# Performance work log

Measured on AMD Instinct MI355X. Metric: run time of the kernel, lower is better.

Reference implementation:

```python
import jax, jax.numpy as jnp
import numpy as np

N_HEAD = 16

def setup_inputs() -> dict:
    key = jax.random.key(0)
    k1, k2, k3 = jax.random.split(key, 3)
    B, T, C = 2, 2048, 1024
    x_norm_for_qk = jax.random.normal(k1, (B, T, C), dtype=jnp.float32)
    xt_current_for_v = jax.random.normal(k2, (B, T, C), dtype=jnp.float32)
    W_attn = jax.random.normal(k3, (C, 2 * C), dtype=jnp.float32) * (1.0 / np.sqrt(C))
    b_attn = jnp.zeros((2 * C,), dtype=jnp.float32)
    return {"x_norm_for_qk": x_norm_for_qk, "xt_current_for_v": xt_current_for_v,
            "W_attn": W_attn, "b_attn": b_attn}

def reference(x_norm_for_qk, xt_current_for_v, W_attn, b_attn):
    B, T, C = x_norm_for_qk.shape
    H = N_HEAD
    D = C // H  # head dim
    qk = x_norm_for_qk @ W_attn + b_attn          # [B,T,2C]
    q, k = qk[..., :C], qk[..., C:]
    q = q.reshape(B, T, H, D).transpose(0, 2, 1, 3)   # [B,H,T,D]
    k = k.reshape(B, T, H, D).transpose(0, 2, 1, 3)
    v = xt_current_for_v.reshape(B, T, H, D).transpose(0, 2, 1, 3)
    scale = 1.0 / np.sqrt(D).astype(np.float32)
    scores = jnp.einsum('bhqd,bhkd->bhqk', q, k) * scale  # [B,H,T,T]
    causal = jnp.tril(jnp.ones((T, T), dtype=bool))
    scores = jnp.where(causal[None, None], scores, jnp.float32(-jnp.inf))
    weights = jax.nn.softmax(scores, axis=-1)  # dropout p=0.0 -> identity
    y = jnp.einsum('bhqk,bhkd->bhqd', weights, v)
    return y.transpose(0, 2, 1, 3).reshape(B, T, C)
```

## Files before the change

kernel.cpp:

```cpp
#include <hip/hip_runtime.h>
#include <hip/hip_bf16.h>
#include <math.h>

typedef __attribute__((ext_vector_type(8))) short s8v;
typedef __attribute__((ext_vector_type(4))) float f4v;
typedef __attribute__((ext_vector_type(16))) float f16v;
typedef __attribute__((ext_vector_type(2))) unsigned int u32x2;
typedef unsigned short ush;
typedef unsigned int u32;

#define QSCALE 0.180336880f
#define FIXED_M 10.0f

static __device__ __forceinline__ ush f2bf(float f) {
    u32 x = __builtin_bit_cast(u32, f);
    return (ush)((x + 0x7fffu + ((x >> 16) & 1u)) >> 16);
}
static __device__ __forceinline__ u32 bfpack(float lo, float hi) {
    u32 a = __builtin_bit_cast(u32, lo) + 0x8000u;
    u32 b = __builtin_bit_cast(u32, hi) + 0x8000u;
    return __builtin_amdgcn_perm(b, a, 0x07060302);
}
static __device__ __forceinline__ void gl_lds16(const void* g, void* l) {
    __builtin_amdgcn_global_load_lds(
        (const __attribute__((address_space(1))) u32*)g,
        (__attribute__((address_space(3))) u32*)l, 16, 0, 0);
}
#if __has_builtin(__builtin_amdgcn_exp2f)
#define EXP2F(x) __builtin_amdgcn_exp2f(x)
#else
#define EXP2F(x) exp2f(x)
#endif

static __device__ __forceinline__ void pl32swap(u32& a, u32& b) {
#if __has_builtin(__builtin_amdgcn_permlane32_swap)
    u32x2 r = __builtin_amdgcn_permlane32_swap(a, b, false, false);
    a = r[0]; b = r[1];
#else
    asm volatile("v_permlane32_swap_b32 %0, %1" : "+v"(a), "+v"(b));
#endif
}
static __device__ __forceinline__ s8v mkfrag(u32 a, u32 b, u32 c, u32 d) {
    union { u32 w[4]; s8v v; } u;
    u.w[0] = a; u.w[1] = b; u.w[2] = c; u.w[3] = d;
    return u.v;
}

__global__ __launch_bounds__(256) void prepA_kernel(
    const float* __restrict__ X, const float* __restrict__ W,
    ush* __restrict__ Xb, ush* __restrict__ Wt)
{
    __shared__ float Ts[64][68];
    const int tid = threadIdx.x;
    const int bid = blockIdx.x;
    if (bid < 2048) {
        const size_t i = ((size_t)bid * 256 + tid) * 8;
        float4 v0 = *(const float4*)(X + i);
        float4 v1 = *(const float4*)(X + i + 4);
        uint4 o;
        o.x = bfpack(v0.x, v0.y); o.y = bfpack(v0.z, v0.w);
        o.z = bfpack(v1.x, v1.y); o.w = bfpack(v1.z, v1.w);
        *(uint4*)(Xb + i) = o;
    } else {
        const int id = bid - 2048;
        const int n0 = (id & 31) * 64, k0 = (id >> 5) * 64;
        #pragma unroll
        for (int p = 0; p < 4; ++p) {
            const int idx = p * 256 + tid;
            const int kr = idx >> 4, nc4 = idx & 15;
            float4 v = *(const float4*)(W + (size_t)(k0 + kr) * 2048 + n0 + nc4 * 4);
            Ts[kr][nc4 * 4 + 0] = v.x; Ts[kr][nc4 * 4 + 1] = v.y;
            Ts[kr][nc4 * 4 + 2] = v.z; Ts[kr][nc4 * 4 + 3] = v.w;
        }
        __syncthreads();
        const int n = tid >> 2, kb = (tid & 3) * 16;
        #pragma unroll
        for (int p = 0; p < 4; ++p) {
            const int k = kb + p * 4;
            ushort4 o;
            o.x = f2bf(Ts[k + 0][n]); o.y = f2bf(Ts[k + 1][n]);
            o.z = f2bf(Ts[k + 2][n]); o.w = f2bf(Ts[k + 3][n]);
            *(ushort4*)(Wt + (size_t)(n0 + n) * 1024 + k0 + k) = o;
        }
    }
}

__global__ __launch_bounds__(256) void vt_kernel(
    const float* __restrict__ XV, ush* __restrict__ Vt)
{
    __shared__ float Ts[64][68];
    const int tid = threadIdx.x;
    const int t0 = blockIdx.x * 64;
    const int bh = blockIdx.y;
    const int b = bh >> 4, h = bh & 15;
    #pragma unroll
    for (int p = 0; p < 4; ++p) {
        const int idx = p * 256 + tid;
        const int tr = idx >> 4, dc4 = idx & 15;
        float4 v = *(const float4*)(XV + (size_t)(b * 2048 + t0 + tr) * 1024
                                    + h * 64 + dc4 * 4);
        Ts[tr][dc4 * 4 + 0] = v.x; Ts[tr][dc4 * 4 + 1] = v.y;
        Ts[tr][dc4 * 4 + 2] = v.z; Ts[tr][dc4 * 4 + 3] = v.w;
    }
    __syncthreads();
    const int d = tid >> 2, tb = (tid & 3) * 16;
    #pragma unroll
    for (int p = 0; p < 4; ++p) {
        const int tq = tb + p * 4;
        ushort4 o;
        o.x = f2bf(Ts[tq + 0][d]); o.y = f2bf(Ts[tq + 1][d]);
        o.z = f2bf(Ts[tq + 2][d]); o.w = f2bf(Ts[tq + 3][d]);
        *(ushort4*)(Vt + (size_t)((b * 16 + h) * 64 + d) * 2048 + t0 + tq) = o;
    }
}

__global__ __launch_bounds__(256) void gemm_kernel(
    const ush* __restrict__ Xb, const ush* __restrict__ Wt,
    const float* __restrict__ bias,
    ush* __restrict__ Qb, ush* __restrict__ Kb)
{
    __shared__ ush As[128 * 32];
    __shared__ ush Bs[128 * 32];

    const int tid = threadIdx.x;
    const int wid = tid >> 6, lane = tid & 63;
    const int quad = lane >> 4, l15 = lane & 15;
    const int wm = wid >> 1, wn = wid & 1;
    const int m0 = blockIdx.y * 128, n0 = blockIdx.x * 128;

    const int lrow = lane >> 2;
    const int lkk = (lane & 3) * 8;
    const size_t arow = (size_t)(m0 + wid * 32 + lrow);
    const size_t brow = (size_t)(n0 + wid * 32 + lrow);
    ush* AsW = &As[wid * 1024];
    ush* BsW = &Bs[wid * 1024];

    f4v acc[4][4];
    #pragma unroll
    for (int i = 0; i < 4; ++i)
        #pragma unroll
        for (int j = 0; j < 4; ++j) acc[i][j] = (f4v){0.f, 0.f, 0.f, 0.f};

    for (int k0 = 0; k0 < 1024; k0 += 32) {
        gl_lds16(Xb + arow * 1024 + k0 + lkk, AsW);
        gl_lds16(Xb + (arow + 16) * 1024 + k0 + lkk, AsW + 512);
        gl_lds16(Wt + brow * 1024 + k0 + lkk, BsW);
        gl_lds16(Wt + (brow + 16) * 1024 + k0 + lkk, BsW + 512);
        __syncthreads();

        s8v a[4], bf[4];
        #pragma unroll
        for (int i = 0; i < 4; ++i)
            a[i] = *(const s8v*)&As[(wm * 64 + i * 16 + l15) * 32 + quad * 8];
        #pragma unroll
        for (int j = 0; j < 4; ++j)
            bf[j] = *(const s8v*)&Bs[(wn * 64 + j * 16 + l15) * 32 + quad * 8];
        #pragma unroll
        for (int i = 0; i < 4; ++i)
            #pragma unroll
            for (int j = 0; j < 4; ++j)
                acc[i][j] = __builtin_amdgcn_mfma_f32_16x16x32_bf16(
                    a[i], bf[j], acc[i][j], 0, 0, 0);
        __syncthreads();
    }

    #pragma unroll
    for (int j = 0; j < 4; ++j) {
        const int n = n0 + wn * 64 + j * 16 + l15;
        const float bv = bias[n];
        const bool is_k = n >= 1024;
        const int nn = n & 1023;
        const int h = nn >> 6, d = nn & 63;
        ush* dst = is_k ? Kb : Qb;
        #pragma unroll
        for (int i = 0; i < 4; ++i) {
            const int mrow = m0 + wm * 64 + i * 16 + quad * 4;
            #pragma unroll
            for (int r = 0; r < 4; ++r) {
                const int m = mrow + r;
                const int b = m >> 11, t = m & 2047;
                float val = acc[i][j][r] + bv;
                if (!is_k) val *= QSCALE;
                dst[(size_t)((b * 16 + h) * 2048 + t) * 64 + d] = f2bf(val);
            }
        }
    }
}

__global__ __launch_bounds__(256, 2) void attn_kernel(
    const ush* __restrict__ Qb, const ush* __restrict__ Kb,
    const ush* __restrict__ Vt, float* __restrict__ Y)
{
    __shared__ ush SMEM[25600];
    ush* Kbuf = SMEM;
    ush* Vbuf = SMEM + 8192;
    ush* Pq   = SMEM + 16384;

    const int tid = threadIdx.x;
    const int w = tid >> 6, lane = tid & 63;
    const int l31 = lane & 31, hi = lane >> 5;

    const int idx = blockIdx.x;
    const int half = idx >> 8, pair = idx & 255;
    const int qt = half ? (pair & 15) : 15 - (pair & 15);
    const int bh = (pair >> 4) + half * 16;
    const int b = bh >> 4, h = bh & 15;
    const int q0 = qt * 128;
    const int ktmax = 2 * qt + 1;

    const ush* Qg = Qb + (size_t)bh * 2048 * 64;
    const ush* Kg = Kb + (size_t)bh * 2048 * 64;
    const ush* Vg = Vt + (size_t)bh * 64 * 2048;

    ush* Pw = Pq + w * 2304;

    {
        const int r8q = lane >> 3, c8 = lane & 7;
        #pragma unroll
        for (int p = 0; p < 4; ++p) {
            const int row = p * 8 + r8q;
            uint4 v = *(const uint4*)(Qg + (size_t)(q0 + w * 32 + row) * 64 + c8 * 8);
            *(uint4*)&Pw[row * 72 + c8 * 8] = v;
        }
    }
    s8v bq[4];
    #pragma unroll
    for (int s = 0; s < 4; ++s)
        bq[s] = *(const s8v*)&Pw[l31 * 72 + s * 16 + hi * 8];

    const int r8 = lane >> 3;
    const int g8 = ((lane & 7) ^ r8) * 8;
    auto stage = [&](int kt, int buf) {
        const int k0e = kt * 64;
        const ush* kg = Kg + (size_t)(k0e + w * 16 + r8) * 64 + g8;
        gl_lds16(kg, &Kbuf[buf * 4096 + (w * 16) * 64]);
        gl_lds16(kg + 8 * 64, &Kbuf[buf * 4096 + (w * 16 + 8) * 64]);
        const ush* vg = Vg + (size_t)(w * 16 + r8) * 2048 + k0e + g8;
        gl_lds16(vg, &Vbuf[buf * 4096 + (w * 16) * 64]);
        gl_lds16(vg + 8 * 2048, &Vbuf[buf * 4096 + (w * 16 + 8) * 64]);
    };

    f16v acco0 = {}, acco1 = {};
    float lr = 0.f;
    const int qg = q0 + w * 32 + l31;
    const int qwmax = q0 + w * 32 + 31;

    stage(0, 0);
    __syncthreads();

    for (int kt = 0; kt <= ktmax; ++kt) {
        const int buf = kt & 1;
        const bool active = (kt * 64) <= qwmax;

        s8v ak0[4], ak1[4], av0[4], av1[4];
        if (active) {
            #pragma unroll
            for (int s = 0; s < 4; ++s) {
                const int ch = (s << 1) + hi;
                const int row0 = l31, row1 = 32 + l31;
                ak0[s] = *(const s8v*)&Kbuf[buf * 4096 + row0 * 64 + ((ch ^ (row0 & 7)) << 3)];
                ak1[s] = *(const s8v*)&Kbuf[buf * 4096 + row1 * 64 + ((ch ^ (row1 & 7)) << 3)];
                av0[s] = *(const s8v*)&Vbuf[buf * 4096 + row0 * 64 + ((ch ^ (row0 & 7)) << 3)];
                av1[s] = *(const s8v*)&Vbuf[buf * 4096 + row1 * 64 + ((ch ^ (row1 & 7)) << 3)];
            }
        }
        __builtin_amdgcn_sched_barrier(0);

        if (kt < ktmax) stage(kt + 1, buf ^ 1);

        if (active) {
            f16v s0 = {}, s1 = {};
            #pragma unroll
            for (int s = 0; s < 4; ++s) {
                s0 = __builtin_amdgcn_mfma_f32_32x32x16_bf16(ak0[s], bq[s], s0, 0, 0, 0);
                s1 = __builtin_amdgcn_mfma_f32_32x32x16_bf16(ak1[s], bq[s], s1, 0, 0, 0);
            }

            float ps = 0.f;
            u32 w0[4], w1[4], x0[4], x1[4];
            const bool needmask = (kt * 64 + 63) > (q0 + w * 32);
            if (needmask) {
                const int kbase = kt * 64 + 4 * hi;
                #pragma unroll
                for (int g4 = 0; g4 < 4; ++g4) {
                    const int kb0 = kbase + 8 * g4;
                    float e0a = (kb0 + 0 > qg) ? 0.f : EXP2F(s0[g4 * 4 + 0] - FIXED_M);
                    float e0b = (kb0 + 1 > qg) ? 0.f : EXP2F(s0[g4 * 4 + 1] - FIXED_M);
                    float e0c = (kb0 + 2 > qg) ? 0.f : EXP2F(s0[g4 * 4 + 2] - FIXED_M);
                    float e0d = (kb0 + 3 > qg) ? 0.f : EXP2F(s0[g4 * 4 + 3] - FIXED_M);
                    float e1a = (kb0 + 32 > qg) ? 0.f : EXP2F(s1[g4 * 4 + 0] - FIXED_M);
                    float e1b = (kb0 + 33 > qg) ? 0.f : EXP2F(s1[g4 * 4 + 1] - FIXED_M);
                    float e1c = (kb0 + 34 > qg) ? 0.f : EXP2F(s1[g4 * 4 + 2] - FIXED_M);
                    float e1d = (kb0 + 35 > qg) ? 0.f : EXP2F(s1[g4 * 4 + 3] - FIXED_M);
                    ps += (e0a + e0b) + (e0c + e0d) + (e1a + e1b) + (e1c + e1d);
                    w0[g4] = bfpack(e0a, e0b); w1[g4] = bfpack(e0c, e0d);
                    x0[g4] = bfpack(e1a, e1b); x1[g4] = bfpack(e1c, e1d);
                }
            } else {
                #pragma unroll
                for (int g4 = 0; g4 < 4; ++g4) {
                    float e0a = EXP2F(s0[g4 * 4 + 0] - FIXED_M);
                    float e0b = EXP2F(s0[g4 * 4 + 1] - FIXED_M);
                    float e0c = EXP2F(s0[g4 * 4 + 2] - FIXED_M);
                    float e0d = EXP2F(s0[g4 * 4 + 3] - FIXED_M);
                    float e1a = EXP2F(s1[g4 * 4 + 0] - FIXED_M);
                    float e1b = EXP2F(s1[g4 * 4 + 1] - FIXED_M);
                    float e1c = EXP2F(s1[g4 * 4 + 2] - FIXED_M);
                    float e1d = EXP2F(s1[g4 * 4 + 3] - FIXED_M);
                    ps += (e0a + e0b) + (e0c + e0d) + (e1a + e1b) + (e1c + e1d);
                    w0[g4] = bfpack(e0a, e0b); w1[g4] = bfpack(e0c, e0d);
                    x0[g4] = bfpack(e1a, e1b); x1[g4] = bfpack(e1c, e1d);
                }
            }
            ps += __shfl_xor(ps, 32);
            lr += ps;

            pl32swap(w0[0], w0[1]); pl32swap(w1[0], w1[1]);
            pl32swap(w0[2], w0[3]); pl32swap(w1[2], w1[3]);
            pl32swap(x0[0], x0[1]); pl32swap(x1[0], x1[1]);
            pl32swap(x0[2], x0[3]); pl32swap(x1[2], x1[3]);
            s8v pf0 = mkfrag(w0[0], w1[0], w0[1], w1[1]);
            s8v pf1 = mkfrag(w0[2], w1[2], w0[3], w1[3]);
            s8v pf2 = mkfrag(x0[0], x1[0], x0[1], x1[1]);
            s8v pf3 = mkfrag(x0[2], x1[2], x0[3], x1[3]);

            acco0 = __builtin_amdgcn_mfma_f32_32x32x16_bf16(av0[0], pf0, acco0, 0, 0, 0);
            acco1 = __builtin_amdgcn_mfma_f32_32x32x16_bf16(av1[0], pf0, acco1, 0, 0, 0);
            acco0 = __builtin_amdgcn_mfma_f32_32x32x16_bf16(av0[1], pf1, acco0, 0, 0, 0);
            acco1 = __builtin_amdgcn_mfma_f32_32x32x16_bf16(av1[1], pf1, acco1, 0, 0, 0);
            acco0 = __builtin_amdgcn_mfma_f32_32x32x16_bf16(av0[2], pf2, acco0, 0, 0, 0);
            acco1 = __builtin_amdgcn_mfma_f32_32x32x16_bf16(av1[2], pf2, acco1, 0, 0, 0);
            acco0 = __builtin_amdgcn_mfma_f32_32x32x16_bf16(av0[3], pf3, acco0, 0, 0, 0);
            acco1 = __builtin_amdgcn_mfma_f32_32x32x16_bf16(av1[3], pf3, acco1, 0, 0, 0);
        }

        __syncthreads();
    }

    __syncthreads();
    float* LTw = (float*)SMEM + w * (32 * 68);
    const float inv = 1.0f / lr;
    #pragma unroll
    for (int r = 0; r < 16; ++r) {
        const int d = (r & 3) + 8 * (r >> 2) + 4 * hi;
        LTw[l31 * 68 + d] = acco0[r] * inv;
        LTw[l31 * 68 + 32 + d] = acco1[r] * inv;
    }
    const int qr4 = lane >> 4, chk = lane & 15;
    #pragma unroll
    for (int p = 0; p < 8; ++p) {
        const int qrow = p * 4 + qr4;
        f4v v = *(const f4v*)&LTw[qrow * 68 + chk * 4];
        *(float4*)(Y + (size_t)(b * 2048 + q0 + w * 32 + qrow) * 1024
                   + h * 64 + chk * 4) = (float4){v[0], v[1], v[2], v[3]};
    }
}

extern "C" void kernel_launch(void* const* d_in, const int* in_sizes, int n_in,
                              void* d_out, int out_size, void* d_ws,
                              size_t ws_size, hipStream_t stream)
{
    const float* x_qk = (const float*)d_in[0];
    const float* x_v  = (const float*)d_in[1];
    const float* W    = (const float*)d_in[2];
    const float* bias = (const float*)d_in[3];
    float* out = (float*)d_out;

    unsigned char* ws = (unsigned char*)d_ws;
    ush* Xb = (ush*)(ws);
    ush* Vt = (ush*)(ws);
    ush* Wt = (ush*)(ws + (8u << 20));
    ush* Qb = (ush*)(ws + (12u << 20));
    ush* Kb = (ush*)(ws + (20u << 20));

    prepA_kernel<<<2560, 256, 0, stream>>>(x_qk, W, Xb, Wt);
    gemm_kernel<<<dim3(16, 32), 256, 0, stream>>>(Xb, Wt, bias, Qb, Kb);
    vt_kernel<<<dim3(32, 32), 256, 0, stream>>>(x_v, Vt);
    attn_kernel<<<512, 256, 0, stream>>>(Qb, Kb, Vt, out);
}
```

Before: 151.1 us.

## Process two KV tiles per attention iteration with 4-slot staging; fuse V transpose into prep

The attention loop now handles two 64-key tiles per iteration. It uses a 4-slot LDS ring (64KB shared) that prefetches the next two tiles, and keeps separate accumulators per tile so their MFMA chains are independent and there is one barrier per pair of tiles. Q staging now reuses the K buffer region, which needs an extra barrier. The V transpose kernel is merged into the prep kernel with its own workspace region, removing one launch. The changes raise register and LDS use, which may lower occupancy below the 2 blocks per CU requested by launch_bounds.

Result: slower. 212.6 us (+40.7%).

```diff
diff --git a/kernel.cpp b/kernel.cpp
--- a/kernel.cpp
+++ b/kernel.cpp
@@ -46,9 +46,60 @@
     return u.v;
 }
 
-__global__ __launch_bounds__(256) void prepA_kernel(
+static __device__ __forceinline__ void softpack(
+    const f16v& s0, const f16v& s1, bool needmask, int kbase, int qg,
+    float& lr, s8v& pf0, s8v& pf1, s8v& pf2, s8v& pf3)
+{
+    float ps = 0.f;
+    u32 w0[4], w1[4], x0[4], x1[4];
+    if (needmask) {
+        #pragma unroll
+        for (int g4 = 0; g4 < 4; ++g4) {
+            const int kb0 = kbase + 8 * g4;
+            float e0a = (kb0 + 0 > qg) ? 0.f : EXP2F(s0[g4 * 4 + 0] - FIXED_M);
+            float e0b = (kb0 + 1 > qg) ? 0.f : EXP2F(s0[g4 * 4 + 1] - FIXED_M);
+            float e0c = (kb0 + 2 > qg) ? 0.f : EXP2F(s0[g4 * 4 + 2] - FIXED_M);
+            float e0d = (kb0 + 3 > qg) ? 0.f : EXP2F(s0[g4 * 4 + 3] - FIXED_M);
+            float e1a = (kb0 + 32 > qg) ? 0.f : EXP2F(s1[g4 * 4 + 0] - FIXED_M);
+            float e1b = (kb0 + 33 > qg) ? 0.f : EXP2F(s1[g4 * 4 + 1] - FIXED_M);
+            float e1c = (kb0 + 34 > qg) ? 0.f : EXP2F(s1[g4 * 4 + 2] - FIXED_M);
+            float e1d = (kb0 + 35 > qg) ? 0.f : EXP2F(s1[g4 * 4 + 3] - FIXED_M);
+            ps += (e0a + e0b) + (e0c + e0d) + (e1a + e1b) + (e1c + e1d);
+            w0[g4] = bfpack(e0a, e0b); w1[g4] = bfpack(e0c, e0d);
+            x0[g4] = bfpack(e1a, e1b); x1[g4] = bfpack(e1c, e1d);
+        }
+    } else {
+        #pragma unroll
+        for (int g4 = 0; g4 < 4; ++g4) {
+            float e0a = EXP2F(s0[g4 * 4 + 0] - FIXED_M);
+            float e0b = EXP2F(s0[g4 * 4 + 1] - FIXED_M);
+            float e0c = EXP2F(s0[g4 * 4 + 2] - FIXED_M);
+            float e0d = EXP2F(s0[g4 * 4 + 3] - FIXED_M);
+            float e1a = EXP2F(s1[g4 * 4 + 0] - FIXED_M);
+            float e1b = EXP2F(s1[g4 * 4 + 1] - FIXED_M);
+            float e1c = EXP2F(s1[g4 * 4 + 2] - FIXED_M);
+            float e1d = EXP2F(s1[g4 * 4 + 3] - FIXED_M);
+            ps += (e0a + e0b) + (e0c + e0d) + (e1a + e1b) + (e1c + e1d);
+            w0[g4] = bfpack(e0a, e0b); w1[g4] = bfpack(e0c, e0d);
+            x0[g4] = bfpack(e1a, e1b); x1[g4] = bfpack(e1c, e1d);
+        }
+    }
+    ps += __shfl_xor(ps, 32);
+    lr += ps;
+    pl32swap(w0[0], w0[1]); pl32swap(w1[0], w1[1]);
+    pl32swap(w0[2], w0[3]); pl32swap(w1[2], w1[3]);
+    pl32swap(x0[0], x0[1]); pl32swap(x1[0], x1[1]);
+    pl32swap(x0[2], x0[3]); pl32swap(x1[2], x1[3]);
+    pf0 = mkfrag(w0[0], w1[0], w0[1], w1[1]);
+    pf1 = mkfrag(w0[2], w1[2], w0[3], w1[3]);
+    pf2 = mkfrag(x0[0], x1[0], x0[1], x1[1]);
+    pf3 = mkfrag(x0[2], x1[2], x0[3], x1[3]);
+}
+
+__global__ __launch_bounds__(256) void prep_kernel(
     const float* __restrict__ X, const float* __restrict__ W,
-    ush* __restrict__ Xb, ush* __restrict__ Wt)
+    const float* __restrict__ XV,
+    ush* __restrict__ Xb, ush* __restrict__ Wt, ush* __restrict__ Vtb)
 {
     __shared__ float Ts[64][68];
     const int tid = threadIdx.x;
@@ -61,7 +112,7 @@
         o.x = bfpack(v0.x, v0.y); o.y = bfpack(v0.z, v0.w);
         o.z = bfpack(v1.x, v1.y); o.w = bfpack(v1.z, v1.w);
         *(uint4*)(Xb + i) = o;
-    } else {
+    } else if (bid < 2560) {
         const int id = bid - 2048;
         const int n0 = (id & 31) * 64, k0 = (id >> 5) * 64;
         #pragma unroll
@@ -82,35 +133,30 @@
             o.z = f2bf(Ts[k + 2][n]); o.w = f2bf(Ts[k + 3][n]);
             *(ushort4*)(Wt + (size_t)(n0 + n) * 1024 + k0 + k) = o;
         }
-    }
-}
-
-__global__ __launch_bounds__(256) void vt_kernel(
-    const float* __restrict__ XV, ush* __restrict__ Vt)
-{
-    __shared__ float Ts[64][68];
-    const int tid = threadIdx.x;
-    const int t0 = blockIdx.x * 64;
-    const int bh = blockIdx.y;
-    const int b = bh >> 4, h = bh & 15;
-    #pragma unroll
-    for (int p = 0; p < 4; ++p) {
-        const int idx = p * 256 + tid;
-        const int tr = idx >> 4, dc4 = idx & 15;
-        float4 v = *(const float4*)(XV + (size_t)(b * 2048 + t0 + tr) * 1024
-                                    + h * 64 + dc4 * 4);
-        Ts[tr][dc4 * 4 + 0] = v.x; Ts[tr][dc4 * 4 + 1] = v.y;
-        Ts[tr][dc4 * 4 + 2] = v.z; Ts[tr][dc4 * 4 + 3] = v.w;
-    }
-    __syncthreads();
-    const int d = tid >> 2, tb = (tid & 3) * 16;
-    #pragma unroll
-    for (int p = 0; p < 4; ++p) {
-        const int tq = tb + p * 4;
-        ushort4 o;
-        o.x = f2bf(Ts[tq + 0][d]); o.y = f2bf(Ts[tq + 1][d]);
-        o.z = f2bf(Ts[tq + 2][d]); o.w = f2bf(Ts[tq + 3][d]);
-        *(ushort4*)(Vt + (size_t)((b * 16 + h) * 64 + d) * 2048 + t0 + tq) = o;
+    } else {
+        const int id = bid - 2560;
+        const int t0 = (id & 31) * 64;
+        const int bh = id >> 5;
+        const int b = bh >> 4, h = bh & 15;
+        #pragma unroll
+        for (int p = 0; p < 4; ++p) {
+            const int idx = p * 256 + tid;
+            const int tr = idx >> 4, dc4 = idx & 15;
+            float4 v = *(const float4*)(XV + (size_t)(b * 2048 + t0 + tr) * 1024
+                                        + h * 64 + dc4 * 4);
+            Ts[tr][dc4 * 4 + 0] = v.x; Ts[tr][dc4 * 4 + 1] = v.y;
+            Ts[tr][dc4 * 4 + 2] = v.z; Ts[tr][dc4 * 4 + 3] = v.w;
+        }
+        __syncthreads();
+        const int d = tid >> 2, tb = (tid & 3) * 16;
+        #pragma unroll
+        for (int p = 0; p < 4; ++p) {
+            const int tq = tb + p * 4;
+            ushort4 o;
+            o.x = f2bf(Ts[tq + 0][d]); o.y = f2bf(Ts[tq + 1][d]);
+            o.z = f2bf(Ts[tq + 2][d]); o.w = f2bf(Ts[tq + 3][d]);
+            *(ushort4*)(Vtb + (size_t)((b * 16 + h) * 64 + d) * 2048 + t0 + tq) = o;
+        }
     }
 }
 
@@ -191,10 +237,9 @@
     const ush* __restrict__ Qb, const ush* __restrict__ Kb,
     const ush* __restrict__ Vt, float* __restrict__ Y)
 {
-    __shared__ ush SMEM[25600];
+    __shared__ ush SMEM[32768];
     ush* Kbuf = SMEM;
-    ush* Vbuf = SMEM + 8192;
-    ush* Pq   = SMEM + 16384;
+    ush* Vbuf = SMEM + 16384;
 
     const int tid = threadIdx.x;
     const int w = tid >> 6, lane = tid & 63;
@@ -212,8 +257,7 @@
     const ush* Kg = Kb + (size_t)bh * 2048 * 64;
     const ush* Vg = Vt + (size_t)bh * 64 * 2048;
 
-    ush* Pw = Pq + w * 2304;
-
+    ush* Pw = SMEM + w * 2304;
     {
         const int r8q = lane >> 3, c8 = lane & 7;
         #pragma unroll
@@ -227,10 +271,12 @@
     #pragma unroll
     for (int s = 0; s < 4; ++s)
         bq[s] = *(const s8v*)&Pw[l31 * 72 + s * 16 + hi * 8];
+    __syncthreads();
 
     const int r8 = lane >> 3;
     const int g8 = ((lane & 7) ^ r8) * 8;
-    auto stage = [&](int kt, int buf) {
+    auto stage = [&](int kt) {
+        const int buf = kt & 3;
         const int k0e = kt * 64;
         const ush* kg = Kg + (size_t)(k0e + w * 16 + r8) * 64 + g8;
         gl_lds16(kg, &Kbuf[buf * 4096 + (w * 16) * 64]);
@@ -240,98 +286,104 @@
         gl_lds16(vg + 8 * 2048, &Vbuf[buf * 4096 + (w * 16 + 8) * 64]);
     };
 
-    f16v acco0 = {}, acco1 = {};
+    f16v accA0 = {}, accA1 = {}, accB0 = {}, accB1 = {};
     float lr = 0.f;
     const int qg = q0 + w * 32 + l31;
     const int qwmax = q0 + w * 32 + 31;
 
-    stage(0, 0);
+    stage(0); stage(1);
     __syncthreads();
 
-    for (int kt = 0; kt <= ktmax; ++kt) {
-        const int buf = kt & 1;
-        const bool active = (kt * 64) <= qwmax;
-
-        s8v ak0[4], ak1[4], av0[4], av1[4];
-        if (active) {
+    for (int i = 0; i <= qt; ++i) {
+        const int ktA = 2 * i, ktB = 2 * i + 1;
+        const int slA = (ktA & 3) * 4096, slB = (ktB & 3) * 4096;
+        const bool actA = (ktA * 64) <= qwmax;
+        const bool actB = (ktB * 64) <= qwmax;
+
+        s8v akA0[4], akA1[4], akB0[4], akB1[4];
+        if (actA) {
             #pragma unroll
             for (int s = 0; s < 4; ++s) {
                 const int ch = (s << 1) + hi;
                 const int row0 = l31, row1 = 32 + l31;
-                ak0[s] = *(const s8v*)&Kbuf[buf * 4096 + row0 * 64 + ((ch ^ (row0 & 7)) << 3)];
-                ak1[s] = *(const s8v*)&Kbuf[buf * 4096 + row1 * 64 + ((ch ^ (row1 & 7)) << 3)];
-                av0[s] = *(const s8v*)&Vbuf[buf * 4096 + row0 * 64 + ((ch ^ (row0 & 7)) << 3)];
-                av1[s] = *(const s8v*)&Vbuf[buf * 4096 + row1 * 64 + ((ch ^ (row1 & 7)) << 3)];
+                akA0[s] = *(const s8v*)&Kbuf[slA + row0 * 64 + ((ch ^ (row0 & 7)) << 3)];
+                akA1[s] = *(const s8v*)&Kbuf[slA + row1 * 64 + ((ch ^ (row1 & 7)) << 3)];
+            }
+        }
+        if (actB) {
+            #pragma unroll
+            for (int s = 0; s < 4; ++s) {
+                const int ch = (s << 1) + hi;
+                const int row0 = l31, row1 = 32 + l31;
+                akB0[s] = *(const s8v*)&Kbuf[slB + row0 * 64 + ((ch ^ (row0 & 7)) << 3)];
+                akB1[s] = *(const s8v*)&Kbuf[slB + row1 * 64 + ((ch ^ (row1 & 7)) << 3)];
             }
         }
         __builtin_amdgcn_sched_barrier(0);
 
-        if (kt < ktmax) stage(kt + 1, buf ^ 1);
-
-        if (active) {
-            f16v s0 = {}, s1 = {};
-            #pragma unroll
-            for (int s = 0; s < 4; ++s) {
-                s0 = __builtin_amdgcn_mfma_f32_32x32x16_bf16(ak0[s], bq[s], s0, 0, 0, 0);
-                s1 = __builtin_amdgcn_mfma_f32_32x32x16_bf16(ak1[s], bq[s], s1, 0, 0, 0);
-            }
-
-            float ps = 0.f;
-            u32 w0[4], w1[4], x0[4], x1[4];
-            const bool needmask = (kt * 64 + 63) > (q0 + w * 32);
-            if (needmask) {
-                const int kbase = kt * 64 + 4 * hi;
-                #pragma unroll
-                for (int g4 = 0; g4 < 4; ++g4) {
-                    const int kb0 = kbase + 8 * g4;
-                    float e0a = (kb0 + 0 > qg) ? 0.f : EXP2F(s0[g4 * 4 + 0] - FIXED_M);
-                    float e0b = (kb0 + 1 > qg) ? 0.f : EXP2F(s0[g4 * 4 + 1] - FIXED_M);
-                    float e0c = (kb0 + 2 > qg) ? 0.f : EXP2F(s0[g4 * 4 + 2] - FIXED_M);
-                    float e0d = (kb0 + 3 > qg) ? 0.f : EXP2F(s0[g4 * 4 + 3] - FIXED_M);
-                    float e1a = (kb0 + 32 > qg) ? 0.f : EXP2F(s1[g4 * 4 + 0] - FIXED_M);
-                    float e1b = (kb0 + 33 > qg) ? 0.f : EXP2F(s1[g4 * 4 + 1] - FIXED_M);
-                    float e1c = (kb0 + 34 > qg) ? 0.f : EXP2F(s1[g4 * 4 + 2] - FIXED_M);
-                    float e1d = (kb0 + 35 > qg) ? 0.f : EXP2F(s1[g4 * 4 + 3] - FIXED_M);
-                    ps += (e0a + e0b) + (e0c + e0d) + (e1a + e1b) + (e1c + e1d);
-                    w0[g4] = bfpack(e0a, e0b); w1[g4] = bfpack(e0c, e0d);
-                    x0[g4] = bfpack(e1a, e1b); x1[g4] = bfpack(e1c, e1d);
-                }
-            } else {
-                #pragma unroll
-                for (int g4 = 0; g4 < 4; ++g4) {
-                    float e0a = EXP2F(s0[g4 * 4 + 0] - FIXED_M);
-                    float e0b = EXP2F(s0[g4 * 4 + 1] - FIXED_M);
-                    float e0c = EXP2F(s0[g4 * 4 + 2] - FIXED_M);
-                    float e0d = EXP2F(s0[g4 * 4 + 3] - FIXED_M);
-                    float e1a = EXP2F(s1[g4 * 4 + 0] - FIXED_M);
-                    float e1b = EXP2F(s1[g4 * 4 + 1] - FIXED_M);
-                    float e1c = EXP2F(s1[g4 * 4 + 2] - FIXED_M);
-                    float e1d = EXP2F(s1[g4 * 4 + 3] - FIXED_M);
-                    ps += (e0a + e0b) + (e0c + e0d) + (e1a + e1b) + (e1c + e1d);
-                    w0[g4] = bfpack(e0a, e0b); w1[g4] = bfpack(e0c, e0d);
-                    x0[g4] = bfpack(e1a, e1b); x1[g4] = bfpack(e1c, e1d);
-                }
-            }
-            ps += __shfl_xor(ps, 32);
-            lr += ps;
-
-            pl32swap(w0[0], w0[1]); pl32swap(w1[0], w1[1]);
-            pl32swap(w0[2], w0[3]); pl32swap(w1[2], w1[3]);
-            pl32swap(x0[0], x0[1]); pl32swap(x1[0], x1[1]);
-            pl32swap(x0[2], x0[3]); pl32swap(x1[2], x1[3]);
-            s8v pf0 = mkfrag(w0[0], w1[0], w0[1], w1[1]);
-            s8v pf1 = mkfrag(w0[2], w1[2], w0[3], w1[3]);
-            s8v pf2 = mkfrag(x0[0], x1[0], x0[1], x1[1]);
-            s8v pf3 = mkfrag(x0[2], x1[2], x0[3], x1[3]);
-
-            acco0 = __builtin_amdgcn_mfma_f32_32x32x16_bf16(av0[0], pf0, acco0, 0, 0, 0);
-            acco1 = __builtin_amdgcn_mfma_f32_32x32x16_bf16(av1[0], pf0, acco1, 0, 0, 0);
-            acco0 = __builtin_amdgcn_mfma_f32_32x32x16_bf16(av0[1], pf1, acco0, 0, 0, 0);
-            acco1 = __builtin_amdgcn_mfma_f32_32x32x16_bf16(av1[1], pf1, acco1, 0, 0, 0);
-            acco0 = __builtin_amdgcn_mfma_f32_32x32x16_bf16(av0[2], pf2, acco0, 0, 0, 0);
-            acco1 = __builtin_amdgcn_mfma_f32_32x32x16_bf16(av1[2], pf2, acco1, 0, 0, 0);
-            acco0 = __builtin_amdgcn_mfma_f32_32x32x16_bf16(av0[3], pf3, acco0, 0, 0, 0);
-            acco1 = __builtin_amdgcn_mfma_f32_32x32x16_bf16(av1[3], pf3, acco1, 0, 0, 0);
+        if (i < qt) { stage(ktA + 2); stage(ktB + 2); }
+
+        f16v s0A = {}, s1A = {}, s0B = {}, s1B = {};
+        if (actA) {
+            #pragma unroll
+            for (int s = 0; s < 4; ++s) {
+                s0A = __builtin_amdgcn_mfma_f32_32x32x16_bf16(akA0[s], bq[s], s0A, 0, 0, 0);
+                s1A = __builtin_amdgcn_mfma_f32_32x32x16_bf16(akA1[s], bq[s], s1A, 0, 0, 0);
+            }
+        }
+        if (actB) {
+            #pragma unroll
+            for (int s = 0; s < 4; ++s) {
+                s0B = __builtin_amdgcn_mfma_f32_32x32x16_bf16(akB0[s], bq[s], s0B, 0, 0, 0);
+                s1B = __builtin_amdgcn_mfma_f32_32x32x16_bf16(akB1[s], bq[s], s1B, 0, 0, 0);
+            }
+        }
+
+        s8v avA0[4], avA1[4], avB0[4], avB1[4];
+        if (actA) {
+            #pragma unroll
+            for (int s = 0; s < 4; ++s) {
+                const int ch = (s << 1) + hi;
+                const int row0 = l31, row1 = 32 + l31;
+                avA0[s] = *(const s8v*)&Vbuf[slA + row0 * 64 + ((ch ^ (row0 & 7)) << 3)];
+                avA1[s] = *(const s8v*)&Vbuf[slA + row1 * 64 + ((ch ^ (row1 & 7)) << 3)];
+            }
+        }
+        if (actB) {
+            #pragma unroll
+            for (int s = 0; s < 4; ++s) {
+                const int ch = (s << 1) + hi;
+                const int row0 = l31, row1 = 32 + l31;
+                avB0[s] = *(const s8v*)&Vbuf[slB + row0 * 64 + ((ch ^ (row0 & 7)) << 3)];
+                avB1[s] = *(const s8v*)&Vbuf[slB + row1 * 64 + ((ch ^ (row1 & 7)) << 3)];
+            }
+        }
+
+        if (actA) {
+            s8v pf0, pf1, pf2, pf3;
+            softpack(s0A, s1A, (ktA * 64 + 63) > (q0 + w * 32),
+                     ktA * 64 + 4 * hi, qg, lr, pf0, pf1, pf2, pf3);
+            accA0 = __builtin_amdgcn_mfma_f32_32x32x16_bf16(avA0[0], pf0, accA0, 0, 0, 0);
+            accA1 = __builtin_amdgcn_mfma_f32_32x32x16_bf16(avA1[0], pf0, accA1, 0, 0, 0);
+            accA0 = __builtin_amdgcn_mfma_f32_32x32x16_bf16(avA0[1], pf1, accA0, 0, 0, 0);
+            accA1 = __builtin_amdgcn_mfma_f32_32x32x16_bf16(avA1[1], pf1, accA1, 0, 0, 0);
+            accA0 = __builtin_amdgcn_mfma_f32_32x32x16_bf16(avA0[2], pf2, accA0, 0, 0, 0);
+            accA1 = __builtin_amdgcn_mfma_f32_32x32x16_bf16(avA1[2], pf2, accA1, 0, 0, 0);
+            accA0 = __builtin_amdgcn_mfma_f32_32x32x16_bf16(avA0[3], pf3, accA0, 0, 0, 0);
+            accA1 = __builtin_amdgcn_mfma_f32_32x32x16_bf16(avA1[3], pf3, accA1, 0, 0, 0);
+        }
+        if (actB) {
+            s8v pf0, pf1, pf2, pf3;
+            softpack(s0B, s1B, (ktB * 64 + 63) > (q0 + w * 32),
+                     ktB * 64 + 4 * hi, qg, lr, pf0, pf1, pf2, pf3);
+            accB0 = __builtin_amdgcn_mfma_f32_32x32x16_bf16(avB0[0], pf0, accB0, 0, 0, 0);
+            accB1 = __builtin_amdgcn_mfma_f32_32x32x16_bf16(avB1[0], pf0, accB1, 0, 0, 0);
+            accB0 = __builtin_amdgcn_mfma_f32_32x32x16_bf16(avB0[1], pf1, accB0, 0, 0, 0);
+            accB1 = __builtin_amdgcn_mfma_f32_32x32x16_bf16(avB1[1], pf1, accB1, 0, 0, 0);
+            accB0 = __builtin_amdgcn_mfma_f32_32x32x16_bf16(avB0[2], pf2, accB0, 0, 0, 0);
+            accB1 = __builtin_amdgcn_mfma_f32_32x32x16_bf16(avB1[2], pf2, accB1, 0, 0, 0);
+            accB0 = __builtin_amdgcn_mfma_f32_32x32x16_bf16(avB0[3], pf3, accB0, 0, 0, 0);
+            accB1 = __builtin_amdgcn_mfma_f32_32x32x16_bf16(avB1[3], pf3, accB1, 0, 0, 0);
         }
 
         __syncthreads();
@@ -343,8 +395,8 @@
     #pragma unroll
     for (int r = 0; r < 16; ++r) {
         const int d = (r & 3) + 8 * (r >> 2) + 4 * hi;
-        LTw[l31 * 68 + d] = acco0[r] * inv;
-        LTw[l31 * 68 + 32 + d] = acco1[r] * inv;
+        LTw[l31 * 68 + d] = (accA0[r] + accB0[r]) * inv;
+        LTw[l31 * 68 + 32 + d] = (accA1[r] + accB1[r]) * inv;
     }
     const int qr4 = lane >> 4, chk = lane & 15;
     #pragma unroll
@@ -368,13 +420,12 @@
 
     unsigned char* ws = (unsigned char*)d_ws;
     ush* Xb = (ush*)(ws);
-    ush* Vt = (ush*)(ws);
     ush* Wt = (ush*)(ws + (8u << 20));
     ush* Qb = (ush*)(ws + (12u << 20));
     ush* Kb = (ush*)(ws + (20u << 20));
-
-    prepA_kernel<<<2560, 256, 0, stream>>>(x_qk, W, Xb, Wt);
+    ush* Vt = (ush*)(ws + (28u << 20));
+
+    prep_kernel<<<3584, 256, 0, stream>>>(x_qk, W, x_v, Xb, Wt, Vt);
     gemm_kernel<<<dim3(16, 32), 256, 0, stream>>>(Xb, Wt, bias, Qb, Kb);
-    vt_kernel<<<dim3(32, 32), 256, 0, stream>>>(x_v, Vt);
     attn_kernel<<<512, 256, 0, stream>>>(Qb, Kb, Vt, out);
 }
```

## Quad-buffer K/V tiles with two-ahead prefetch and fuse V transpose into prep

Applied to the files above, without the earlier changes.

The attention kernel moves from double-buffered K/V staging with a full __syncthreads per iteration to a 4-slot ring with a prefetch distance of two. Each iteration waits only on the older loads (vmcnt) before a raw s_barrier, so more load latency is hidden at the cost of more shared memory, which can reduce occupancy. The V-transpose kernel is merged into the prep kernel, with V now in its own workspace region instead of aliasing Xb, which removes one launch and lets the V conversion run alongside the X/W conversion. The softmax packing is also moved into a helper function without changing its behaviour.

Result: no change. 148.7 us (-1.6%).

```diff
diff --git a/kernel.cpp b/kernel.cpp
--- a/kernel.cpp
+++ b/kernel.cpp
@@ -46,9 +46,60 @@
     return u.v;
 }
 
-__global__ __launch_bounds__(256) void prepA_kernel(
+static __device__ __forceinline__ void softpack(
+    const f16v& s0, const f16v& s1, bool needmask, int kbase, int qg,
+    float& lr, s8v& pf0, s8v& pf1, s8v& pf2, s8v& pf3)
+{
+    float ps = 0.f;
+    u32 w0[4], w1[4], x0[4], x1[4];
+    if (needmask) {
+        #pragma unroll
+        for (int g4 = 0; g4 < 4; ++g4) {
+            const int kb0 = kbase + 8 * g4;
+            float e0a = (kb0 + 0 > qg) ? 0.f : EXP2F(s0[g4 * 4 + 0] - FIXED_M);
+            float e0b = (kb0 + 1 > qg) ? 0.f : EXP2F(s0[g4 * 4 + 1] - FIXED_M);
+            float e0c = (kb0 + 2 > qg) ? 0.f : EXP2F(s0[g4 * 4 + 2] - FIXED_M);
+            float e0d = (kb0 + 3 > qg) ? 0.f : EXP2F(s0[g4 * 4 + 3] - FIXED_M);
+            float e1a = (kb0 + 32 > qg) ? 0.f : EXP2F(s1[g4 * 4 + 0] - FIXED_M);
+            float e1b = (kb0 + 33 > qg) ? 0.f : EXP2F(s1[g4 * 4 + 1] - FIXED_M);
+            float e1c = (kb0 + 34 > qg) ? 0.f : EXP2F(s1[g4 * 4 + 2] - FIXED_M);
+            float e1d = (kb0 + 35 > qg) ? 0.f : EXP2F(s1[g4 * 4 + 3] - FIXED_M);
+            ps += (e0a + e0b) + (e0c + e0d) + (e1a + e1b) + (e1c + e1d);
+            w0[g4] = bfpack(e0a, e0b); w1[g4] = bfpack(e0c, e0d);
+            x0[g4] = bfpack(e1a, e1b); x1[g4] = bfpack(e1c, e1d);
+        }
+    } else {
+        #pragma unroll
+        for (int g4 = 0; g4 < 4; ++g4) {
+            float e0a = EXP2F(s0[g4 * 4 + 0] - FIXED_M);
+            float e0b = EXP2F(s0[g4 * 4 + 1] - FIXED_M);
+            float e0c = EXP2F(s0[g4 * 4 + 2] - FIXED_M);
+            float e0d = EXP2F(s0[g4 * 4 + 3] - FIXED_M);
+            float e1a = EXP2F(s1[g4 * 4 + 0] - FIXED_M);
+            float e1b = EXP2F(s1[g4 * 4 + 1] - FIXED_M);
+            float e1c = EXP2F(s1[g4 * 4 + 2] - FIXED_M);
+            float e1d = EXP2F(s1[g4 * 4 + 3] - FIXED_M);
+            ps += (e0a + e0b) + (e0c + e0d) + (e1a + e1b) + (e1c + e1d);
+            w0[g4] = bfpack(e0a, e0b); w1[g4] = bfpack(e0c, e0d);
+            x0[g4] = bfpack(e1a, e1b); x1[g4] = bfpack(e1c, e1d);
+        }
+    }
+    ps += __shfl_xor(ps, 32);
+    lr += ps;
+    pl32swap(w0[0], w0[1]); pl32swap(w1[0], w1[1]);
+    pl32swap(w0[2], w0[3]); pl32swap(w1[2], w1[3]);
+    pl32swap(x0[0], x0[1]); pl32swap(x1[0], x1[1]);
+    pl32swap(x0[2], x0[3]); pl32swap(x1[2], x1[3]);
+    pf0 = mkfrag(w0[0], w1[0], w0[1], w1[1]);
+    pf1 = mkfrag(w0[2], w1[2], w0[3], w1[3]);
+    pf2 = mkfrag(x0[0], x1[0], x0[1], x1[1]);
+    pf3 = mkfrag(x0[2], x1[2], x0[3], x1[3]);
+}
+
+__global__ __launch_bounds__(256) void prep_kernel(
     const float* __restrict__ X, const float* __restrict__ W,
-    ush* __restrict__ Xb, ush* __restrict__ Wt)
+    const float* __restrict__ XV,
+    ush* __restrict__ Xb, ush* __restrict__ Wt, ush* __restrict__ Vtb)
 {
     __shared__ float Ts[64][68];
     const int tid = threadIdx.x;
@@ -61,7 +112,7 @@
         o.x = bfpack(v0.x, v0.y); o.y = bfpack(v0.z, v0.w);
         o.z = bfpack(v1.x, v1.y); o.w = bfpack(v1.z, v1.w);
         *(uint4*)(Xb + i) = o;
-    } else {
+    } else if (bid < 2560) {
         const int id = bid - 2048;
         const int n0 = (id & 31) * 64, k0 = (id >> 5) * 64;
         #pragma unroll
@@ -82,35 +133,30 @@
             o.z = f2bf(Ts[k + 2][n]); o.w = f2bf(Ts[k + 3][n]);
             *(ushort4*)(Wt + (size_t)(n0 + n) * 1024 + k0 + k) = o;
         }
-    }
-}
-
-__global__ __launch_bounds__(256) void vt_kernel(
-    const float* __restrict__ XV, ush* __restrict__ Vt)
-{
-    __shared__ float Ts[64][68];
-    const int tid = threadIdx.x;
-    const int t0 = blockIdx.x * 64;
-    const int bh = blockIdx.y;
-    const int b = bh >> 4, h = bh & 15;
-    #pragma unroll
-    for (int p = 0; p < 4; ++p) {
-        const int idx = p * 256 + tid;
-        const int tr = idx >> 4, dc4 = idx & 15;
-        float4 v = *(const float4*)(XV + (size_t)(b * 2048 + t0 + tr) * 1024
-                                    + h * 64 + dc4 * 4);
-        Ts[tr][dc4 * 4 + 0] = v.x; Ts[tr][dc4 * 4 + 1] = v.y;
-        Ts[tr][dc4 * 4 + 2] = v.z; Ts[tr][dc4 * 4 + 3] = v.w;
-    }
-    __syncthreads();
-    const int d = tid >> 2, tb = (tid & 3) * 16;
-    #pragma unroll
-    for (int p = 0; p < 4; ++p) {
-        const int tq = tb + p * 4;
-        ushort4 o;
-        o.x = f2bf(Ts[tq + 0][d]); o.y = f2bf(Ts[tq + 1][d]);
-        o.z = f2bf(Ts[tq + 2][d]); o.w = f2bf(Ts[tq + 3][d]);
-        *(ushort4*)(Vt + (size_t)((b * 16 + h) * 64 + d) * 2048 + t0 + tq) = o;
+    } else {
+        const int id = bid - 2560;
+        const int t0 = (id & 31) * 64;
+        const int bh = id >> 5;
+        const int b = bh >> 4, h = bh & 15;
+        #pragma unroll
+        for (int p = 0; p < 4; ++p) {
+            const int idx = p * 256 + tid;
+            const int tr = idx >> 4, dc4 = idx & 15;
+            float4 v = *(const float4*)(XV + (size_t)(b * 2048 + t0 + tr) * 1024
+                                        + h * 64 + dc4 * 4);
+            Ts[tr][dc4 * 4 + 0] = v.x; Ts[tr][dc4 * 4 + 1] = v.y;
+            Ts[tr][dc4 * 4 + 2] = v.z; Ts[tr][dc4 * 4 + 3] = v.w;
+        }
+        __syncthreads();
+        const int d = tid >> 2, tb = (tid & 3) * 16;
+        #pragma unroll
+        for (int p = 0; p < 4; ++p) {
+            const int tq = tb + p * 4;
+            ushort4 o;
+            o.x = f2bf(Ts[tq + 0][d]); o.y = f2bf(Ts[tq + 1][d]);
+            o.z = f2bf(Ts[tq + 2][d]); o.w = f2bf(Ts[tq + 3][d]);
+            *(ushort4*)(Vtb + (size_t)((b * 16 + h) * 64 + d) * 2048 + t0 + tq) = o;
+        }
     }
 }
 
@@ -191,10 +237,9 @@
     const ush* __restrict__ Qb, const ush* __restrict__ Kb,
     const ush* __restrict__ Vt, float* __restrict__ Y)
 {
-    __shared__ ush SMEM[25600];
+    __shared__ ush SMEM[32768];
     ush* Kbuf = SMEM;
-    ush* Vbuf = SMEM + 8192;
-    ush* Pq   = SMEM + 16384;
+    ush* Vbuf = SMEM + 16384;
 
     const int tid = threadIdx.x;
     const int w = tid >> 6, lane = tid & 63;
@@ -212,8 +257,7 @@
     const ush* Kg = Kb + (size_t)bh * 2048 * 64;
     const ush* Vg = Vt + (size_t)bh * 64 * 2048;
 
-    ush* Pw = Pq + w * 2304;
-
+    ush* Pw = SMEM + w * 2304;
     {
         const int r8q = lane >> 3, c8 = lane & 7;
         #pragma unroll
@@ -227,10 +271,12 @@
     #pragma unroll
     for (int s = 0; s < 4; ++s)
         bq[s] = *(const s8v*)&Pw[l31 * 72 + s * 16 + hi * 8];
+    __syncthreads();
 
     const int r8 = lane >> 3;
     const int g8 = ((lane & 7) ^ r8) * 8;
-    auto stage = [&](int kt, int buf) {
+    auto stage = [&](int kt) {
+        const int buf = kt & 3;
         const int k0e = kt * 64;
         const ush* kg = Kg + (size_t)(k0e + w * 16 + r8) * 64 + g8;
         gl_lds16(kg, &Kbuf[buf * 4096 + (w * 16) * 64]);
@@ -245,12 +291,15 @@
     const int qg = q0 + w * 32 + l31;
     const int qwmax = q0 + w * 32 + 31;
 
-    stage(0, 0);
-    __syncthreads();
+    stage(0); stage(1);
+    asm volatile("s_waitcnt vmcnt(4)" ::: "memory");
+    __builtin_amdgcn_s_barrier();
+    __builtin_amdgcn_sched_barrier(0);
 
     for (int kt = 0; kt <= ktmax; ++kt) {
-        const int buf = kt & 1;
+        const int sl = (kt & 3) * 4096;
         const bool active = (kt * 64) <= qwmax;
+        const bool pf = (kt + 2 <= ktmax);
 
         s8v ak0[4], ak1[4], av0[4], av1[4];
         if (active) {
@@ -258,15 +307,15 @@
             for (int s = 0; s < 4; ++s) {
                 const int ch = (s << 1) + hi;
                 const int row0 = l31, row1 = 32 + l31;
-                ak0[s] = *(const s8v*)&Kbuf[buf * 4096 + row0 * 64 + ((ch ^ (row0 & 7)) << 3)];
-                ak1[s] = *(const s8v*)&Kbuf[buf * 4096 + row1 * 64 + ((ch ^ (row1 & 7)) << 3)];
-                av0[s] = *(const s8v*)&Vbuf[buf * 4096 + row0 * 64 + ((ch ^ (row0 & 7)) << 3)];
-                av1[s] = *(const s8v*)&Vbuf[buf * 4096 + row1 * 64 + ((ch ^ (row1 & 7)) << 3)];
+                ak0[s] = *(const s8v*)&Kbuf[sl + row0 * 64 + ((ch ^ (row0 & 7)) << 3)];
+                ak1[s] = *(const s8v*)&Kbuf[sl + row1 * 64 + ((ch ^ (row1 & 7)) << 3)];
+                av0[s] = *(const s8v*)&Vbuf[sl + row0 * 64 + ((ch ^ (row0 & 7)) << 3)];
+                av1[s] = *(const s8v*)&Vbuf[sl + row1 * 64 + ((ch ^ (row1 & 7)) << 3)];
             }
         }
         __builtin_amdgcn_sched_barrier(0);
 
-        if (kt < ktmax) stage(kt + 1, buf ^ 1);
+        if (pf) stage(kt + 2);
 
         if (active) {
             f16v s0 = {}, s1 = {};
@@ -276,53 +325,9 @@
                 s1 = __builtin_amdgcn_mfma_f32_32x32x16_bf16(ak1[s], bq[s], s1, 0, 0, 0);
             }
 
-            float ps = 0.f;
-            u32 w0[4], w1[4], x0[4], x1[4];
-            const bool needmask = (kt * 64 + 63) > (q0 + w * 32);
-            if (needmask) {
-                const int kbase = kt * 64 + 4 * hi;
-                #pragma unroll
-                for (int g4 = 0; g4 < 4; ++g4) {
-                    const int kb0 = kbase + 8 * g4;
-                    float e0a = (kb0 + 0 > qg) ? 0.f : EXP2F(s0[g4 * 4 + 0] - FIXED_M);
-                    float e0b = (kb0 + 1 > qg) ? 0.f : EXP2F(s0[g4 * 4 + 1] - FIXED_M);
-                    float e0c = (kb0 + 2 > qg) ? 0.f : EXP2F(s0[g4 * 4 + 2] - FIXED_M);
-                    float e0d = (kb0 + 3 > qg) ? 0.f : EXP2F(s0[g4 * 4 + 3] - FIXED_M);
-                    float e1a = (kb0 + 32 > qg) ? 0.f : EXP2F(s1[g4 * 4 + 0] - FIXED_M);
-                    float e1b = (kb0 + 33 > qg) ? 0.f : EXP2F(s1[g4 * 4 + 1] - FIXED_M);
-                    float e1c = (kb0 + 34 > qg) ? 0.f : EXP2F(s1[g4 * 4 + 2] - FIXED_M);
-                    float e1d = (kb0 + 35 > qg) ? 0.f : EXP2F(s1[g4 * 4 + 3] - FIXED_M);
-                    ps += (e0a + e0b) + (e0c + e0d) + (e1a + e1b) + (e1c + e1d);
-                    w0[g4] = bfpack(e0a, e0b); w1[g4] = bfpack(e0c, e0d);
-                    x0[g4] = bfpack(e1a, e1b); x1[g4] = bfpack(e1c, e1d);
-                }
-            } else {
-                #pragma unroll
-                for (int g4 = 0; g4 < 4; ++g4) {
-                    float e0a = EXP2F(s0[g4 * 4 + 0] - FIXED_M);
-                    float e0b = EXP2F(s0[g4 * 4 + 1] - FIXED_M);
-                    float e0c = EXP2F(s0[g4 * 4 + 2] - FIXED_M);
-                    float e0d = EXP2F(s0[g4 * 4 + 3] - FIXED_M);
-                    float e1a = EXP2F(s1[g4 * 4 + 0] - FIXED_M);
-                    float e1b = EXP2F(s1[g4 * 4 + 1] - FIXED_M);
-                    float e1c = EXP2F(s1[g4 * 4 + 2] - FIXED_M);
-                    float e1d = EXP2F(s1[g4 * 4 + 3] - FIXED_M);
-                    ps += (e0a + e0b) + (e0c + e0d) + (e1a + e1b) + (e1c + e1d);
-                    w0[g4] = bfpack(e0a, e0b); w1[g4] = bfpack(e0c, e0d);
-                    x0[g4] = bfpack(e1a, e1b); x1[g4] = bfpack(e1c, e1d);
-                }
-            }
-            ps += __shfl_xor(ps, 32);
-            lr += ps;
-
-            pl32swap(w0[0], w0[1]); pl32swap(w1[0], w1[1]);
-            pl32swap(w0[2], w0[3]); pl32swap(w1[2], w1[3]);
-            pl32swap(x0[0], x0[1]); pl32swap(x1[0], x1[1]);
-            pl32swap(x0[2], x0[3]); pl32swap(x1[2], x1[3]);
-            s8v pf0 = mkfrag(w0[0], w1[0], w0[1], w1[1]);
-            s8v pf1 = mkfrag(w0[2], w1[2], w0[3], w1[3]);
-            s8v pf2 = mkfrag(x0[0], x1[0], x0[1], x1[1]);
-            s8v pf3 = mkfrag(x0[2], x1[2], x0[3], x1[3]);
+            s8v pf0, pf1, pf2, pf3;
+            softpack(s0, s1, (kt * 64 + 63) > (q0 + w * 32),
+                     kt * 64 + 4 * hi, qg, lr, pf0, pf1, pf2, pf3);
 
             acco0 = __builtin_amdgcn_mfma_f32_32x32x16_bf16(av0[0], pf0, acco0, 0, 0, 0);
             acco1 = __builtin_amdgcn_mfma_f32_32x32x16_bf16(av1[0], pf0, acco1, 0, 0, 0);
@@ -334,10 +339,12 @@
             acco1 = __builtin_amdgcn_mfma_f32_32x32x16_bf16(av1[3], pf3, acco1, 0, 0, 0);
         }
 
-        __syncthreads();
-    }
-
-    __syncthreads();
+        if (pf) asm volatile("s_waitcnt vmcnt(4)" ::: "memory");
+        else    asm volatile("s_waitcnt vmcnt(0)" ::: "memory");
+        __builtin_amdgcn_s_barrier();
+        __builtin_amdgcn_sched_barrier(0);
+    }
+
     float* LTw = (float*)SMEM + w * (32 * 68);
     const float inv = 1.0f / lr;
     #pragma unroll
@@ -368,13 +375,12 @@
 
     unsigned char* ws = (unsigned char*)d_ws;
     ush* Xb = (ush*)(ws);
-    ush* Vt = (ush*)(ws);
     ush* Wt = (ush*)(ws + (8u << 20));
     ush* Qb = (ush*)(ws + (12u << 20));
     ush* Kb = (ush*)(ws + (20u << 20));
-
-    prepA_kernel<<<2560, 256, 0, stream>>>(x_qk, W, Xb, Wt);
+    ush* Vt = (ush*)(ws + (28u << 20));
+
+    prep_kernel<<<3584, 256, 0, stream>>>(x_qk, W, x_v, Xb, Wt, Vt);
     gemm_kernel<<<dim3(16, 32), 256, 0, stream>>>(Xb, Wt, bias, Qb, Kb);
-    vt_kernel<<<dim3(32, 32), 256, 0, stream>>>(x_v, Vt);
     attn_kernel<<<512, 256, 0, stream>>>(Qb, Kb, Vt, out);
 }
```
